# Kernel tuning notes

Measured on AMD Instinct MI355X. Metric: run time of the kernel, lower is better.

The kernel has to match this reference:

```python
import jax, jax.numpy as jnp
import numpy as np

D = 1024        # d_group
H = 8           # num_heads_group
WIN = 128       # attention window size
DH = D // H     # head_dim = 128
EPS = 1e-5


def _rmsnorm(x, scale):
    xf = x.astype(jnp.float32)
    var = jnp.mean(jnp.square(xf), axis=-1, keepdims=True)
    return (xf * jax.lax.rsqrt(var + EPS) * scale.astype(jnp.float32)).astype(x.dtype)


def _rope(x):
    # x: [B', S, H, Dh]
    S, Dh = x.shape[1], x.shape[3]
    freqs = 1.0 / (10000.0 ** (jnp.arange(0, Dh, 2, dtype=jnp.float32) / Dh))
    ang = jnp.arange(S, dtype=jnp.float32)[:, None] * freqs[None, :]  # [S, Dh/2]
    sin = jnp.repeat(jnp.sin(ang), 2, axis=-1)[None, :, None, :]
    cos = jnp.repeat(jnp.cos(ang), 2, axis=-1)[None, :, None, :]
    x1, x2 = jnp.split(x, 2, axis=-1)
    rot = jnp.concatenate([-x2, x1], axis=-1)
    return x * cos + rot * sin


def setup_inputs() -> dict:
    key = jax.random.key(0)
    ks = jax.random.split(key, 16)
    s = 0.02
    return {
        "group_x": jax.random.normal(ks[0], (8, 4096, D), jnp.float32),
        "context": jax.random.normal(ks[1], (8, D), jnp.float32),
        "W_ada": jax.random.normal(ks[2], (D, 6 * D), jnp.float32) * s,
        "b_ada": jnp.zeros((6 * D,), jnp.float32),
        "scale1": jnp.ones((D,), jnp.float32),
        "W_qkv": jax.random.normal(ks[3], (D, 3 * D), jnp.float32) * s,
        "b_qkv": jnp.zeros((3 * D,), jnp.float32),
        "W_out": jax.random.normal(ks[4], (D, D), jnp.float32) * s,
        "b_out": jnp.zeros((D,), jnp.float32),
        "scale2": jnp.ones((D,), jnp.float32),
        "W_ff1": jax.random.normal(ks[5], (D, 4 * D), jnp.float32) * s,
        "b_ff1": jnp.zeros((4 * D,), jnp.float32),
        "W_ff2": jax.random.normal(ks[6], (4 * D, D), jnp.float32) * s,
        "b_ff2": jnp.zeros((D,), jnp.float32),
    }


def reference(group_x, context, W_ada, b_ada, scale1, W_qkv, b_qkv, W_out, b_out,
              scale2, W_ff1, b_ff1, W_ff2, b_ff2):
    B, L, _ = group_x.shape
    nw = L // WIN

    # adaLN modulation params from context
    ada = jax.nn.silu(context) @ W_ada + b_ada              # [B, 6D]
    sh_msa, sc_msa, g_msa, sh_mlp, sc_mlp, g_mlp = jnp.split(ada, 6, axis=-1)
    sh_msa, sc_msa, g_msa = sh_msa[:, None], sc_msa[:, None], g_msa[:, None]
    sh_mlp, sc_mlp, g_mlp = sh_mlp[:, None], sc_mlp[:, None], g_mlp[:, None]

    # --- attention branch ---
    res = group_x
    x = _rmsnorm(group_x, scale1)
    x = x * (1 + sc_msa) + sh_msa
    xw = x.reshape(B * nw, WIN, D)
    qkv = xw @ W_qkv + b_qkv
    q, k, v = jnp.split(qkv, 3, axis=-1)
    q = _rope(q.reshape(B * nw, WIN, H, DH))
    k = _rope(k.reshape(B * nw, WIN, H, DH))
    v = v.reshape(B * nw, WIN, H, DH)
    scores = jnp.einsum('bqhd,bkhd->bhqk', q, k) / jnp.sqrt(jnp.float32(DH))
    attn = jax.nn.softmax(scores, axis=-1)
    o = jnp.einsum('bhqk,bkhd->bqhd', attn, v).reshape(B, L, D)
    o = o @ W_out + b_out
    x = res + g_msa * o

    # --- MLP branch ---
    res = x
    h = _rmsnorm(x, scale2)
    h = h * (1 + sc_mlp) + sh_mlp
    h = jax.nn.gelu(h @ W_ff1 + b_ff1)
    h = h @ W_ff2 + b_ff2
    return res + g_mlp * h
```

## Files before the change

### kernel.cpp

```cpp
#include <hip/hip_runtime.h>
#include <cstdint>
#include <cstddef>

typedef __bf16 bf16;
typedef __bf16 bf16x2 __attribute__((ext_vector_type(2)));
typedef __bf16 bf16x4 __attribute__((ext_vector_type(4)));
typedef __bf16 bf16x8 __attribute__((ext_vector_type(8)));
typedef float f32x4 __attribute__((ext_vector_type(4)));

#define D_MODEL 1024
#define ADA_STRIDE 6144
#define ROWS_TOTAL 32768
#define EPS_RMS 1e-5f

__device__ __forceinline__ void gld16(const void* g, void* l) {
  __builtin_amdgcn_global_load_lds((const __attribute__((address_space(1))) void*)g,
                                   (__attribute__((address_space(3))) void*)l, 16, 0, 0);
}

__global__ void wconvert_t(const float* __restrict__ W, bf16* __restrict__ Wt,
                           int kbits, int N, int total) {
  int i = blockIdx.x * 256 + threadIdx.x;
  if (i >= total) return;
  int K = 1 << kbits;
  int k = i & (K - 1);
  int n = i >> kbits;
  Wt[i] = (bf16)W[(size_t)k * N + n];
}

__global__ void ada_gemm(const float* __restrict__ ctx, const float* __restrict__ W,
                         const float* __restrict__ bias, float* __restrict__ ada) {
  __shared__ float sc[D_MODEL];
  int b = blockIdx.y;
  int col = blockIdx.x * 256 + threadIdx.x;
  for (int j = threadIdx.x; j < D_MODEL; j += 256) {
    float x = ctx[b * D_MODEL + j];
    sc[j] = x / (1.f + __expf(-x));
  }
  __syncthreads();
  float acc = bias[col];
#pragma unroll 8
  for (int k = 0; k < D_MODEL; ++k)
    acc += sc[k] * W[(size_t)k * ADA_STRIDE + col];
  ada[b * ADA_STRIDE + col] = acc;
}

__global__ void rmsnorm_mod(const float* __restrict__ x, const float* __restrict__ scale,
                            const float* __restrict__ ada, int shOff, int scOff,
                            bf16* __restrict__ out) {
  int row = blockIdx.x;
  int b = row >> 12;
  int t = threadIdx.x;
  const float* xr = x + (size_t)row * D_MODEL;
  float4 v = ((const float4*)xr)[t];
  float ss = v.x * v.x + v.y * v.y + v.z * v.z + v.w * v.w;
#pragma unroll
  for (int m = 32; m >= 1; m >>= 1) ss += __shfl_xor(ss, m, 64);
  __shared__ float ws[4];
  if ((t & 63) == 0) ws[t >> 6] = ss;
  __syncthreads();
  float tot = ws[0] + ws[1] + ws[2] + ws[3];
  float rms = rsqrtf(tot * (1.f / D_MODEL) + EPS_RMS);
  const float* ab = ada + b * ADA_STRIDE;
  int d0 = t * 4;
  float vv[4] = {v.x, v.y, v.z, v.w};
  bf16x4 o4;
#pragma unroll
  for (int j = 0; j < 4; ++j) {
    int d = d0 + j;
    float y = vv[j] * rms * scale[d];
    y = y * (1.f + ab[scOff + d]) + ab[shOff + d];
    o4[j] = (bf16)y;
  }
  *(bf16x4*)(out + (size_t)row * D_MODEL + d0) = o4;
}

__global__ void rope_kernel(bf16* __restrict__ qk) {
  int gid = blockIdx.x * 256 + threadIdx.x;
  int t = gid >> 5, i = gid & 31;
  int pos = t & 127;
  float fl = __expf((float)i * -0.14391156831f);
  float al = (float)pos * fl, ah = al * 0.01f;
  float sl, cl, sh, ch;
  __sincosf(al, &sl, &cl);
  __sincosf(ah, &sh, &ch);
  bf16* row = qk + (size_t)t * 2048;
  int d0 = i * 2;
#pragma unroll
  for (int h8 = 0; h8 < 16; ++h8) {
    bf16* hp = row + h8 * 128;
    bf16x2 lo = *(bf16x2*)(hp + d0);
    bf16x2 hi = *(bf16x2*)(hp + 64 + d0);
    bf16x2 olo, ohi;
#pragma unroll
    for (int j = 0; j < 2; ++j) {
      float xl = (float)lo[j], xh = (float)hi[j];
      olo[j] = (bf16)(xl * cl - xh * sl);
      ohi[j] = (bf16)(xh * ch + xl * sh);
    }
    *(bf16x2*)(hp + d0) = olo;
    *(bf16x2*)(hp + 64 + d0) = ohi;
  }
}

#define GEMM_LDS 131072

#define VMWAIT(N) asm volatile("s_waitcnt vmcnt(" #N ")" ::: "memory")
#define PH_BAR() __builtin_amdgcn_s_barrier()
#define KT_DO(...) __VA_ARGS__
#define KT_SKIP(...)

#define READ_AE() { _Pragma("unroll") for (int m_ = 0; m_ < 4; ++m_) \
  _Pragma("unroll") for (int s_ = 0; s_ < 2; ++s_) \
    a[m_][s_] = *(const bf16x8*)(lds + cb + aRow + m_ * 2048 + (g0 ^ (s_ * 32))); }
#define READ_AO() { _Pragma("unroll") for (int m_ = 0; m_ < 4; ++m_) \
  _Pragma("unroll") for (int s_ = 0; s_ < 2; ++s_) \
    a[m_][s_] = *(const bf16x8*)(lds + cb + aRow + 1024 + m_ * 2048 + (g0 ^ (s_ * 32))); }
#define READ_BE() { _Pragma("unroll") for (int n_ = 0; n_ < 2; ++n_) \
  _Pragma("unroll") for (int s_ = 0; s_ < 2; ++s_) \
    be[n_][s_] = *(const bf16x8*)(lds + cb + bRow + n_ * 2048 + (g0 ^ (s_ * 32))); }
#define READ_BO() { _Pragma("unroll") for (int n_ = 0; n_ < 2; ++n_) \
  _Pragma("unroll") for (int s_ = 0; s_ < 2; ++s_) \
    bo[n_][s_] = *(const bf16x8*)(lds + cb + bRow + 1024 + n_ * 2048 + (g0 ^ (s_ * 32))); }

#define MMPH(MOFF, BREG, NOFF) { __builtin_amdgcn_s_setprio(1); \
  _Pragma("unroll") for (int m_ = 0; m_ < 4; ++m_) \
  _Pragma("unroll") for (int n_ = 0; n_ < 2; ++n_) \
  _Pragma("unroll") for (int s_ = 0; s_ < 2; ++s_) \
    acc[2 * m_ + (MOFF)][2 * n_ + (NOFF)] = __builtin_amdgcn_mfma_f32_16x16x32_bf16( \
        BREG[n_][s_], a[m_][s_], acc[2 * m_ + (MOFF)][2 * n_ + (NOFF)], 0, 0, 0); \
  __builtin_amdgcn_s_setprio(0); }

#define KTILE(W0, W1, W2, STG) { \
    VMWAIT(W0); PH_BAR(); \
    READ_AE(); READ_BE(); \
    STG(gld16(gA + ko2, ldAn); gld16(gA + ko2 + K8, ldAn + 512);) \
    MMPH(0, be, 0); \
    VMWAIT(W1); PH_BAR(); \
    READ_BO(); \
    STG(gld16(gB + ko2, ldBn); gld16(gB + ko2 + K8, ldBn + 512);) \
    MMPH(0, bo, 1); \
    VMWAIT(W2); PH_BAR(); \
    READ_AO(); \
    STG(gld16(gB + ko2 + K16, ldBn + 1024); gld16(gB + ko2 + K24, ldBn + 1536);) \
    MMPH(1, bo, 1); \
    PH_BAR(); \
    STG(gld16(gA + ko2 + K16, ldAn + 1024); gld16(gA + ko2 + K24, ldAn + 1536);) \
    MMPH(1, be, 0); \
  }

template <int EPI>
__global__ __launch_bounds__(512, 2) void gemm256(
    const bf16* __restrict__ A, const bf16* __restrict__ Bt,
    const float* __restrict__ bias, int M, int K, int N,
    bf16* __restrict__ outB, float* __restrict__ outF,
    const float* __restrict__ resid, const float* __restrict__ ada, int gOff) {
  extern __shared__ char smem_raw[];
  bf16* lds = (bf16*)smem_raw;
  const int tid = threadIdx.x;
  const int lane = tid & 63;
  const int wv = tid >> 6;
  const int wm = wv >> 2;
  const int wn = wv & 3;
  const int lm = lane & 15;
  const int quad = lane >> 4;

  const int MT = M >> 8, NT = N >> 8;
  const int nwg = MT * NT;
  const int bid = blockIdx.x;
  const int wgid = (bid & 7) * (nwg >> 3) + (bid >> 3);
  const int width = 8 * NT;
  const int gid = wgid / width;
  const int first = gid * 8;
  const int gsize = (MT - first < 8) ? (MT - first) : 8;
  const int inG = wgid % width;
  const int tileM = (first + inG % gsize) << 8;
  const int tileN = (inG / gsize) << 8;

  const int srow = 32 * (tid >> 6) + ((tid & 63) >> 3);
  const int xg = ((tid & 7) ^ ((tid >> 3) & 7)) * 8;
  const bf16* gA = A + (size_t)(tileM + srow) * K + xg;
  const bf16* gB = Bt + (size_t)(tileN + srow) * K + xg;
  const size_t K8 = (size_t)K * 8;
  const size_t K16 = K8 * 2, K24 = K8 * 3;
  bf16* ldA = lds + (tid >> 6) * 2048 + (tid & 63) * 8;
  bf16* ldB = ldA + 16384;

  f32x4 acc[8][4];
#pragma unroll
  for (int i = 0; i < 8; ++i)
#pragma unroll
    for (int j = 0; j < 4; ++j) acc[i][j] = (f32x4){0.f, 0.f, 0.f, 0.f};

  const int g0 = (quad ^ (lm & 7)) * 8;
  const int aRow = wm * 8192 + lm * 64;
  const int bRow = 16384 + wn * 4096 + lm * 64;

  bf16x8 a[4][2], be[2][2], bo[2][2];

  gld16(gA, ldA);        gld16(gA + K8, ldA + 512);
  gld16(gB, ldB);        gld16(gB + K8, ldB + 512);
  gld16(gB + K16, ldB + 1024); gld16(gB + K24, ldB + 1536);
  gld16(gA + K16, ldA + 1024); gld16(gA + K24, ldA + 1536);

  const int nt = K >> 6;
  int cb = 0;
  for (int t = 0; t < nt - 1; ++t) {
    bf16* ldAn = ldA + (cb ^ 32768);
    bf16* ldBn = ldB + (cb ^ 32768);
    const size_t ko2 = (size_t)(t + 1) * 64;
    KTILE(4, 4, 4, KT_DO)
    cb ^= 32768;
  }
  KTILE(4, 2, 0, KT_SKIP)

#pragma unroll
  for (int mi = 0; mi < 8; ++mi) {
    int grow = tileM + wm * 128 + mi * 16 + lm;
    int b = grow >> 12;
    float brow = (EPI == 4) ? bias[grow] : 0.f;
#pragma unroll
    for (int ni = 0; ni < 4; ++ni) {
      int col0 = tileN + wn * 64 + ni * 16 + quad * 4;
      size_t idx = (size_t)grow * N + col0;
      if (EPI == 0) {
        float4 b4 = *(const float4*)(bias + col0);
        float bb[4] = {b4.x, b4.y, b4.z, b4.w};
        bf16x4 o;
#pragma unroll
        for (int r = 0; r < 4; ++r) o[r] = (bf16)(acc[mi][ni][r] + bb[r]);
        *(bf16x4*)(outB + idx) = o;
      } else if (EPI == 4) {
        bf16x4 o;
#pragma unroll
        for (int r = 0; r < 4; ++r) o[r] = (bf16)(acc[mi][ni][r] + brow);
        *(bf16x4*)(outB + idx) = o;
      } else if (EPI == 1) {
        float4 b4 = *(const float4*)(bias + col0);
        float bb[4] = {b4.x, b4.y, b4.z, b4.w};
        bf16x4 o;
#pragma unroll
        for (int r = 0; r < 4; ++r) {
          float v = acc[mi][ni][r] + bb[r];
          float s2 = 1.5957691216057308f * (v + 0.044715f * v * v * v);
          o[r] = (bf16)(v / (1.f + __expf(-s2)));
        }
        *(bf16x4*)(outB + idx) = o;
      } else if (EPI == 2) {
        float4 b4 = *(const float4*)(bias + col0);
        float4 g4 = *(const float4*)(ada + b * ADA_STRIDE + gOff + col0);
        float4 r4 = *(const float4*)(resid + idx);
        float4 o4;
        o4.x = r4.x + g4.x * (acc[mi][ni][0] + b4.x);
        o4.y = r4.y + g4.y * (acc[mi][ni][1] + b4.y);
        o4.z = r4.z + g4.z * (acc[mi][ni][2] + b4.z);
        o4.w = r4.w + g4.w * (acc[mi][ni][3] + b4.w);
        *(float4*)(outF + idx) = o4;
      } else {
        float4 b4 = *(const float4*)(bias + col0);
        float4 g4 = *(const float4*)(ada + b * ADA_STRIDE + gOff + col0);
        float4 r4 = *(const float4*)(outF + idx);
        float4 o4;
        o4.x = r4.x + g4.x * (acc[mi][ni][0] + b4.x);
        o4.y = r4.y + g4.y * (acc[mi][ni][1] + b4.y);
        o4.z = r4.z + g4.z * (acc[mi][ni][2] + b4.z);
        o4.w = r4.w + g4.w * (acc[mi][ni][3] + b4.w);
        *(float4*)(outF + idx) = o4;
      }
    }
  }
}

#define ATTN_LDS 65536

__global__ __launch_bounds__(256, 2) void attn_kernel(
    const bf16* __restrict__ qk, const bf16* __restrict__ vt, bf16* __restrict__ o) {
  extern __shared__ char smem[];
  bf16* qbuf = (bf16*)smem;
  bf16* kbuf = qbuf + 128 * 128;
  const int tid = threadIdx.x;
  const int lane = tid & 63;
  const int wv = tid >> 6;
  const int lm = lane & 15;
  const int quad = lane >> 4;
  const int w = blockIdx.x >> 3;
  const int h = blockIdx.x & 7;
  const int wbase = w * 128;

#pragma unroll
  for (int it = 0; it < 8; ++it) {
    int c = it * 256 + tid;
    int r = c >> 4, gst = c & 15;
    int goff = (gst ^ (r & 15)) * 8;
    const bf16* rowp = qk + (size_t)(wbase + r) * 2048 + h * 128 + goff;
    gld16(rowp, qbuf + c * 8);
    gld16(rowp + 1024, kbuf + c * 8);
  }
  __syncthreads();

  const int wq0 = wv * 32;
  f32x4 accS[8][2];
#pragma unroll
  for (int mi = 0; mi < 8; ++mi)
#pragma unroll
    for (int ni = 0; ni < 2; ++ni) accS[mi][ni] = (f32x4){0.f, 0.f, 0.f, 0.f};

#pragma unroll
  for (int s = 0; s < 4; ++s) {
    bf16x8 bq[2], ak[8];
#pragma unroll
    for (int ni = 0; ni < 2; ++ni)
      bq[ni] = *(const bf16x8*)(qbuf + (wq0 + ni * 16 + lm) * 128 + ((s * 4 + quad) ^ lm) * 8);
#pragma unroll
    for (int mi = 0; mi < 8; ++mi)
      ak[mi] = *(const bf16x8*)(kbuf + (mi * 16 + lm) * 128 + ((s * 4 + quad) ^ lm) * 8);
#pragma unroll
    for (int mi = 0; mi < 8; ++mi)
#pragma unroll
      for (int ni = 0; ni < 2; ++ni)
        accS[mi][ni] = __builtin_amdgcn_mfma_f32_16x16x32_bf16(ak[mi], bq[ni], accS[mi][ni], 0, 0, 0);
  }

  const float scl = 0.08838834764831845f;
  float mx[2] = {-1e30f, -1e30f}, sm[2] = {0.f, 0.f};
#pragma unroll
  for (int mi = 0; mi < 8; ++mi)
#pragma unroll
    for (int ni = 0; ni < 2; ++ni)
#pragma unroll
      for (int r = 0; r < 4; ++r) {
        accS[mi][ni][r] *= scl;
        mx[ni] = fmaxf(mx[ni], accS[mi][ni][r]);
      }
#pragma unroll
  for (int ni = 0; ni < 2; ++ni) {
    mx[ni] = fmaxf(mx[ni], __shfl_xor(mx[ni], 16, 64));
    mx[ni] = fmaxf(mx[ni], __shfl_xor(mx[ni], 32, 64));
  }
#pragma unroll
  for (int mi = 0; mi < 8; ++mi)
#pragma unroll
    for (int ni = 0; ni < 2; ++ni)
#pragma unroll
      for (int r = 0; r < 4; ++r) {
        accS[mi][ni][r] = __expf(accS[mi][ni][r] - mx[ni]);
        sm[ni] += accS[mi][ni][r];
      }
#pragma unroll
  for (int ni = 0; ni < 2; ++ni) {
    sm[ni] += __shfl_xor(sm[ni], 16, 64);
    sm[ni] += __shfl_xor(sm[ni], 32, 64);
    sm[ni] = 1.f / sm[ni];
  }
  __syncthreads();

#pragma unroll
  for (int mi = 0; mi < 8; ++mi)
#pragma unroll
    for (int ni = 0; ni < 2; ++ni) {
      int q = wq0 + ni * 16 + lm;
      int gst = (mi * 2 + (quad >> 1)) ^ lm;
      bf16x4 pk;
#pragma unroll
      for (int r = 0; r < 4; ++r) pk[r] = (bf16)(accS[mi][ni][r] * sm[ni]);
      *(bf16x4*)(qbuf + q * 128 + gst * 8 + (quad & 1) * 4) = pk;
    }
#pragma unroll
  for (int it = 0; it < 8; ++it) {
    int c = it * 256 + tid;
    int r = c >> 4, gst = c & 15;
    gld16(vt + (size_t)(h * 128 + r) * 32768 + wbase + (gst ^ (r & 15)) * 8, kbuf + c * 8);
  }
  __syncthreads();

  f32x4 accO[2][8];
#pragma unroll
  for (int mi = 0; mi < 2; ++mi)
#pragma unroll
    for (int ni = 0; ni < 8; ++ni) accO[mi][ni] = (f32x4){0.f, 0.f, 0.f, 0.f};
#pragma unroll
  for (int s = 0; s < 4; ++s) {
    bf16x8 ap[2], bv[8];
#pragma unroll
    for (int mi = 0; mi < 2; ++mi)
      ap[mi] = *(const bf16x8*)(qbuf + (wq0 + mi * 16 + lm) * 128 + ((s * 4 + quad) ^ lm) * 8);
#pragma unroll
    for (int ni = 0; ni < 8; ++ni)
      bv[ni] = *(const bf16x8*)(kbuf + (ni * 16 + lm) * 128 + ((s * 4 + quad) ^ lm) * 8);
#pragma unroll
    for (int mi = 0; mi < 2; ++mi)
#pragma unroll
      for (int ni = 0; ni < 8; ++ni)
        accO[mi][ni] = __builtin_amdgcn_mfma_f32_16x16x32_bf16(ap[mi], bv[ni], accO[mi][ni], 0, 0, 0);
  }

#pragma unroll
  for (int mi = 0; mi < 2; ++mi)
#pragma unroll
    for (int ni = 0; ni < 8; ++ni) {
      int d = ni * 16 + lm;
#pragma unroll
      for (int r = 0; r < 4; ++r) {
        int q = wq0 + mi * 16 + quad * 4 + r;
        o[(size_t)(wbase + q) * 1024 + h * 128 + d] = (bf16)accO[mi][ni][r];
      }
    }
}

extern "C" void kernel_launch(void* const* d_in, const int* in_sizes, int n_in,
                              void* d_out, int out_size, void* d_ws, size_t ws_size,
                              hipStream_t stream) {
  const float* group_x = (const float*)d_in[0];
  const float* context = (const float*)d_in[1];
  const float* W_ada   = (const float*)d_in[2];
  const float* b_ada   = (const float*)d_in[3];
  const float* scale1  = (const float*)d_in[4];
  const float* W_qkv   = (const float*)d_in[5];
  const float* b_qkv   = (const float*)d_in[6];
  const float* W_out   = (const float*)d_in[7];
  const float* b_out   = (const float*)d_in[8];
  const float* scale2  = (const float*)d_in[9];
  const float* W_ff1   = (const float*)d_in[10];
  const float* b_ff1   = (const float*)d_in[11];
  const float* W_ff2   = (const float*)d_in[12];
  const float* b_ff2   = (const float*)d_in[13];
  float* out = (float*)d_out;

  char* ws = (char*)d_ws;
  float* ada   = (float*)ws;
  bf16* wqkv_t = (bf16*)(ws + 196608);
  bf16* wout_t = wqkv_t + (size_t)3072 * 1024;
  bf16* wff1_t = wout_t + (size_t)1024 * 1024;
  bf16* wff2_t = wff1_t + (size_t)4096 * 1024;
  bf16* bufX   = wff2_t + (size_t)1024 * 4096;
  bf16* qkvQK  = bufX + (size_t)ROWS_TOTAL * 1024;
  bf16* vtbuf  = qkvQK + (size_t)ROWS_TOTAL * 2048;
  bf16* h1     = qkvQK;

  wconvert_t<<<dim3(3072 * 1024 / 256), 256, 0, stream>>>(W_qkv, wqkv_t, 10, 3072, 3072 * 1024);
  wconvert_t<<<dim3(1024 * 1024 / 256), 256, 0, stream>>>(W_out, wout_t, 10, 1024, 1024 * 1024);
  wconvert_t<<<dim3(4096 * 1024 / 256), 256, 0, stream>>>(W_ff1, wff1_t, 10, 4096, 4096 * 1024);
  wconvert_t<<<dim3(1024 * 4096 / 256), 256, 0, stream>>>(W_ff2, wff2_t, 12, 1024, 1024 * 4096);

  ada_gemm<<<dim3(ADA_STRIDE / 256, 8), 256, 0, stream>>>(context, W_ada, b_ada, ada);

  rmsnorm_mod<<<ROWS_TOTAL, 256, 0, stream>>>(group_x, scale1, ada, 0, 1024, bufX);

  hipFuncSetAttribute(reinterpret_cast<const void*>(&gemm256<0>),
                      hipFuncAttributeMaxDynamicSharedMemorySize, GEMM_LDS);
  hipFuncSetAttribute(reinterpret_cast<const void*>(&gemm256<1>),
                      hipFuncAttributeMaxDynamicSharedMemorySize, GEMM_LDS);
  hipFuncSetAttribute(reinterpret_cast<const void*>(&gemm256<2>),
                      hipFuncAttributeMaxDynamicSharedMemorySize, GEMM_LDS);
  hipFuncSetAttribute(reinterpret_cast<const void*>(&gemm256<3>),
                      hipFuncAttributeMaxDynamicSharedMemorySize, GEMM_LDS);
  hipFuncSetAttribute(reinterpret_cast<const void*>(&gemm256<4>),
                      hipFuncAttributeMaxDynamicSharedMemorySize, GEMM_LDS);

  gemm256<0><<<dim3(128 * 8), 512, GEMM_LDS, stream>>>(
      bufX, wqkv_t, b_qkv, ROWS_TOTAL, 1024, 2048, qkvQK, nullptr, nullptr, nullptr, 0);

  gemm256<4><<<dim3(4 * 128), 512, GEMM_LDS, stream>>>(
      wqkv_t + (size_t)2048 * 1024, bufX, b_qkv + 2048, 1024, 1024, ROWS_TOTAL,
      vtbuf, nullptr, nullptr, nullptr, 0);

  rope_kernel<<<dim3(ROWS_TOTAL * 32 / 256), 256, 0, stream>>>(qkvQK);

  hipFuncSetAttribute(reinterpret_cast<const void*>(&attn_kernel),
                      hipFuncAttributeMaxDynamicSharedMemorySize, ATTN_LDS);
  attn_kernel<<<dim3(256 * 8), 256, ATTN_LDS, stream>>>(qkvQK, vtbuf, bufX);

  gemm256<2><<<dim3(128 * 4), 512, GEMM_LDS, stream>>>(
      bufX, wout_t, b_out, ROWS_TOTAL, 1024, 1024, nullptr, out, group_x, ada, 2048);

  rmsnorm_mod<<<ROWS_TOTAL, 256, 0, stream>>>(out, scale2, ada, 3072, 4096, bufX);

  gemm256<1><<<dim3(128 * 16), 512, GEMM_LDS, stream>>>(
      bufX, wff1_t, b_ff1, ROWS_TOTAL, 1024, 4096, h1, nullptr, nullptr, nullptr, 0);

  gemm256<3><<<dim3(128 * 4), 512, GEMM_LDS, stream>>>(
      h1, wff2_t, b_ff2, ROWS_TOTAL, 4096, 1024, nullptr, out, nullptr, ada, 5120);
}
```

Baseline: 1.424 ms.

## Make GEMM persistent with cross-tile prefetch overlapping epilogue

```diff
diff --git a/kernel.cpp b/kernel.cpp
--- a/kernel.cpp
+++ b/kernel.cpp
@@ -107,8 +107,6 @@
 
 #define VMWAIT(N) asm volatile("s_waitcnt vmcnt(" #N ")" ::: "memory")
 #define PH_BAR() __builtin_amdgcn_s_barrier()
-#define KT_DO(...) __VA_ARGS__
-#define KT_SKIP(...)
 
 #define READ_AE() { _Pragma("unroll") for (int m_ = 0; m_ < 4; ++m_) \
   _Pragma("unroll") for (int s_ = 0; s_ < 2; ++s_) \
@@ -131,89 +129,50 @@
         BREG[n_][s_], a[m_][s_], acc[2 * m_ + (MOFF)][2 * n_ + (NOFF)], 0, 0, 0); \
   __builtin_amdgcn_s_setprio(0); }
 
-#define KTILE(W0, W1, W2, STG) { \
+#define STG_A01() gld16(gAs + ko2, ldAn); gld16(gAs + ko2 + K8, ldAn + 512)
+#define STG_B01() gld16(gBs + ko2, ldBn); gld16(gBs + ko2 + K8, ldBn + 512)
+#define STG_B23() gld16(gBs + ko2 + K16, ldBn + 1024); gld16(gBs + ko2 + K24, ldBn + 1536)
+#define STG_A23() gld16(gAs + ko2 + K16, ldAn + 1024); gld16(gAs + ko2 + K24, ldAn + 1536)
+
+#define KTILE_BODY(W0, W1, W3, S0, S1, S2, S3) { \
+    READ_AE(); READ_BE(); \
+    S0; \
     VMWAIT(W0); PH_BAR(); \
-    READ_AE(); READ_BE(); \
-    STG(gld16(gA + ko2, ldAn); gld16(gA + ko2 + K8, ldAn + 512);) \
     MMPH(0, be, 0); \
+    PH_BAR(); \
+    READ_BO(); \
+    S1; \
     VMWAIT(W1); PH_BAR(); \
-    READ_BO(); \
-    STG(gld16(gB + ko2, ldBn); gld16(gB + ko2 + K8, ldBn + 512);) \
     MMPH(0, bo, 1); \
-    VMWAIT(W2); PH_BAR(); \
+    PH_BAR(); \
     READ_AO(); \
-    STG(gld16(gB + ko2 + K16, ldBn + 1024); gld16(gB + ko2 + K24, ldBn + 1536);) \
+    S2; \
+    PH_BAR(); \
     MMPH(1, bo, 1); \
     PH_BAR(); \
-    STG(gld16(gA + ko2 + K16, ldAn + 1024); gld16(gA + ko2 + K24, ldAn + 1536);) \
+    S3; \
+    VMWAIT(W3); PH_BAR(); \
     MMPH(1, be, 0); \
-  }
+    PH_BAR(); \
+  }
+
+__device__ __forceinline__ void decode_tile(int vb, int nwg, int MT, int NT,
+                                            int& tileM, int& tileN) {
+  int wgid = (vb & 7) * (nwg >> 3) + (vb >> 3);
+  int width = 8 * NT;
+  int gid = wgid / width;
+  int first = gid * 8;
+  int gsize = (MT - first < 8) ? (MT - first) : 8;
+  int inG = wgid % width;
+  tileM = (first + inG % gsize) << 8;
+  tileN = (inG / gsize) << 8;
+}
 
 template <int EPI>
-__global__ __launch_bounds__(512, 2) void gemm256(
-    const bf16* __restrict__ A, const bf16* __restrict__ Bt,
-    const float* __restrict__ bias, int M, int K, int N,
-    bf16* __restrict__ outB, float* __restrict__ outF,
+__device__ __forceinline__ void epilogue256(
+    f32x4 (&acc)[8][4], int tileM, int tileN, int N, int wm, int wn, int lm, int quad,
+    const float* __restrict__ bias, bf16* __restrict__ outB, float* __restrict__ outF,
     const float* __restrict__ resid, const float* __restrict__ ada, int gOff) {
-  extern __shared__ char smem_raw[];
-  bf16* lds = (bf16*)smem_raw;
-  const int tid = threadIdx.x;
-  const int lane = tid & 63;
-  const int wv = tid >> 6;
-  const int wm = wv >> 2;
-  const int wn = wv & 3;
-  const int lm = lane & 15;
-  const int quad = lane >> 4;
-
-  const int MT = M >> 8, NT = N >> 8;
-  const int nwg = MT * NT;
-  const int bid = blockIdx.x;
-  const int wgid = (bid & 7) * (nwg >> 3) + (bid >> 3);
-  const int width = 8 * NT;
-  const int gid = wgid / width;
-  const int first = gid * 8;
-  const int gsize = (MT - first < 8) ? (MT - first) : 8;
-  const int inG = wgid % width;
-  const int tileM = (first + inG % gsize) << 8;
-  const int tileN = (inG / gsize) << 8;
-
-  const int srow = 32 * (tid >> 6) + ((tid & 63) >> 3);
-  const int xg = ((tid & 7) ^ ((tid >> 3) & 7)) * 8;
-  const bf16* gA = A + (size_t)(tileM + srow) * K + xg;
-  const bf16* gB = Bt + (size_t)(tileN + srow) * K + xg;
-  const size_t K8 = (size_t)K * 8;
-  const size_t K16 = K8 * 2, K24 = K8 * 3;
-  bf16* ldA = lds + (tid >> 6) * 2048 + (tid & 63) * 8;
-  bf16* ldB = ldA + 16384;
-
-  f32x4 acc[8][4];
-#pragma unroll
-  for (int i = 0; i < 8; ++i)
-#pragma unroll
-    for (int j = 0; j < 4; ++j) acc[i][j] = (f32x4){0.f, 0.f, 0.f, 0.f};
-
-  const int g0 = (quad ^ (lm & 7)) * 8;
-  const int aRow = wm * 8192 + lm * 64;
-  const int bRow = 16384 + wn * 4096 + lm * 64;
-
-  bf16x8 a[4][2], be[2][2], bo[2][2];
-
-  gld16(gA, ldA);        gld16(gA + K8, ldA + 512);
-  gld16(gB, ldB);        gld16(gB + K8, ldB + 512);
-  gld16(gB + K16, ldB + 1024); gld16(gB + K24, ldB + 1536);
-  gld16(gA + K16, ldA + 1024); gld16(gA + K24, ldA + 1536);
-
-  const int nt = K >> 6;
-  int cb = 0;
-  for (int t = 0; t < nt - 1; ++t) {
-    bf16* ldAn = ldA + (cb ^ 32768);
-    bf16* ldBn = ldB + (cb ^ 32768);
-    const size_t ko2 = (size_t)(t + 1) * 64;
-    KTILE(4, 4, 4, KT_DO)
-    cb ^= 32768;
-  }
-  KTILE(4, 2, 0, KT_SKIP)
-
 #pragma unroll
   for (int mi = 0; mi < 8; ++mi) {
     int grow = tileM + wm * 128 + mi * 16 + lm;
@@ -271,6 +230,100 @@
   }
 }
 
+template <int EPI>
+__global__ __launch_bounds__(512, 2) void gemm256(
+    const bf16* __restrict__ A, const bf16* __restrict__ Bt,
+    const float* __restrict__ bias, int M, int K, int N,
+    bf16* __restrict__ outB, float* __restrict__ outF,
+    const float* __restrict__ resid, const float* __restrict__ ada, int gOff) {
+  extern __shared__ char smem_raw[];
+  bf16* lds = (bf16*)smem_raw;
+  const int tid = threadIdx.x;
+  const int lane = tid & 63;
+  const int wv = tid >> 6;
+  const int wm = wv >> 2;
+  const int wn = wv & 3;
+  const int lm = lane & 15;
+  const int quad = lane >> 4;
+
+  const int MT = M >> 8, NT = N >> 8;
+  const int nwg = MT * NT;
+  const int nt = K >> 6;
+
+  int vb = blockIdx.x;
+  int tileM, tileN;
+  decode_tile(vb, nwg, MT, NT, tileM, tileN);
+
+  const int srow = 32 * wv + (lane >> 3);
+  const int xg = ((tid & 7) ^ ((tid >> 3) & 7)) * 8;
+  const size_t K8 = (size_t)K * 8;
+  const size_t K16 = K8 * 2, K24 = K8 * 3;
+  const bf16* gA = A + (size_t)(tileM + srow) * K + xg;
+  const bf16* gB = Bt + (size_t)(tileN + srow) * K + xg;
+  bf16* ldA = lds + wv * 2048 + lane * 8;
+  bf16* ldB = ldA + 16384;
+
+  const int g0 = (quad ^ (lm & 7)) * 8;
+  const int aRow = wm * 8192 + lm * 64;
+  const int bRow = 16384 + wn * 4096 + lm * 64;
+
+  f32x4 acc[8][4];
+  bf16x8 a[4][2], be[2][2], bo[2][2];
+
+  {
+    const bf16* gAs = gA; const bf16* gBs = gB;
+    bf16* ldAn = ldA; bf16* ldBn = ldB;
+    const size_t ko2 = 0;
+    STG_A01(); STG_B01(); STG_B23(); STG_A23();
+  }
+  VMWAIT(4);
+  PH_BAR();
+
+  int cb = 0;
+  for (;;) {
+#pragma unroll
+    for (int i = 0; i < 8; ++i)
+#pragma unroll
+      for (int j = 0; j < 4; ++j) acc[i][j] = (f32x4){0.f, 0.f, 0.f, 0.f};
+
+    const int vnext = vb + 256;
+    const bool more = vnext < nwg;
+
+    for (int t = 0; t < nt - 1; ++t) {
+      const bf16* gAs = gA; const bf16* gBs = gB;
+      bf16* ldAn = ldA + (cb ^ 32768);
+      bf16* ldBn = ldB + (cb ^ 32768);
+      const size_t ko2 = (size_t)(t + 1) * 64;
+      KTILE_BODY(4, 4, 4, STG_A01(), STG_B01(), STG_B23(), STG_A23())
+      cb ^= 32768;
+    }
+
+    if (more) {
+      int tileM2, tileN2;
+      decode_tile(vnext, nwg, MT, NT, tileM2, tileN2);
+      const bf16* gA2 = A + (size_t)(tileM2 + srow) * K + xg;
+      const bf16* gB2 = Bt + (size_t)(tileN2 + srow) * K + xg;
+      {
+        const bf16* gAs = gA2; const bf16* gBs = gB2;
+        bf16* ldAn = ldA + (cb ^ 32768);
+        bf16* ldBn = ldB + (cb ^ 32768);
+        const size_t ko2 = 0;
+        KTILE_BODY(4, 4, 4, STG_A01(), STG_B01(), STG_B23(), STG_A23())
+      }
+      cb ^= 32768;
+      epilogue256<EPI>(acc, tileM, tileN, N, wm, wn, lm, quad,
+                       bias, outB, outF, resid, ada, gOff);
+      vb = vnext; tileM = tileM2; tileN = tileN2; gA = gA2; gB = gB2;
+    } else {
+      KTILE_BODY(2, 0, 0, , , , )
+      cb ^= 32768;
+      epilogue256<EPI>(acc, tileM, tileN, N, wm, wn, lm, quad,
+                       bias, outB, outF, resid, ada, gOff);
+      break;
+    }
+  }
+}
+
 #define ATTN_LDS 65536
 
 __global__ __launch_bounds__(256, 2) void attn_kernel(
@@ -457,10 +510,10 @@
   hipFuncSetAttribute(reinterpret_cast<const void*>(&gemm256<4>),
                       hipFuncAttributeMaxDynamicSharedMemorySize, GEMM_LDS);
 
-  gemm256<0><<<dim3(128 * 8), 512, GEMM_LDS, stream>>>(
+  gemm256<0><<<dim3(256), 512, GEMM_LDS, stream>>>(
       bufX, wqkv_t, b_qkv, ROWS_TOTAL, 1024, 2048, qkvQK, nullptr, nullptr, nullptr, 0);
 
-  gemm256<4><<<dim3(4 * 128), 512, GEMM_LDS, stream>>>(
+  gemm256<4><<<dim3(256), 512, GEMM_LDS, stream>>>(
       wqkv_t + (size_t)2048 * 1024, bufX, b_qkv + 2048, 1024, 1024, ROWS_TOTAL,
       vtbuf, nullptr, nullptr, nullptr, 0);
 
@@ -470,14 +523,14 @@
                       hipFuncAttributeMaxDynamicSharedMemorySize, ATTN_LDS);
   attn_kernel<<<dim3(256 * 8), 256, ATTN_LDS, stream>>>(qkvQK, vtbuf, bufX);
 
-  gemm256<2><<<dim3(128 * 4), 512, GEMM_LDS, stream>>>(
+  gemm256<2><<<dim3(256), 512, GEMM_LDS, stream>>>(
       bufX, wout_t, b_out, ROWS_TOTAL, 1024, 1024, nullptr, out, group_x, ada, 2048);
 
   rmsnorm_mod<<<ROWS_TOTAL, 256, 0, stream>>>(out, scale2, ada, 3072, 4096, bufX);
 
-  gemm256<1><<<dim3(128 * 16), 512, GEMM_LDS, stream>>>(
+  gemm256<1><<<dim3(256), 512, GEMM_LDS, stream>>>(
       bufX, wff1_t, b_ff1, ROWS_TOTAL, 1024, 4096, h1, nullptr, nullptr, nullptr, 0);
 
-  gemm256<3><<<dim3(128 * 4), 512, GEMM_LDS, stream>>>(
+  gemm256<3><<<dim3(256), 512, GEMM_LDS, stream>>>(
       h1, wff2_t, b_ff2, ROWS_TOTAL, 4096, 1024, nullptr, out, nullptr, ada, 5120);
 }
```

Measured after the change: 1.489 ms. 1.05x slower.

## Halve barriers per k-tile in the bf16 GEMM by double-buffering A fragments

Applied to the files above, without the earlier changes.

```diff
diff --git a/kernel.cpp b/kernel.cpp
--- a/kernel.cpp
+++ b/kernel.cpp
@@ -107,15 +107,13 @@
 
 #define VMWAIT(N) asm volatile("s_waitcnt vmcnt(" #N ")" ::: "memory")
 #define PH_BAR() __builtin_amdgcn_s_barrier()
-#define KT_DO(...) __VA_ARGS__
-#define KT_SKIP(...)
 
 #define READ_AE() { _Pragma("unroll") for (int m_ = 0; m_ < 4; ++m_) \
   _Pragma("unroll") for (int s_ = 0; s_ < 2; ++s_) \
-    a[m_][s_] = *(const bf16x8*)(lds + cb + aRow + m_ * 2048 + (g0 ^ (s_ * 32))); }
+    ae[m_][s_] = *(const bf16x8*)(lds + cb + aRow + m_ * 2048 + (g0 ^ (s_ * 32))); }
 #define READ_AO() { _Pragma("unroll") for (int m_ = 0; m_ < 4; ++m_) \
   _Pragma("unroll") for (int s_ = 0; s_ < 2; ++s_) \
-    a[m_][s_] = *(const bf16x8*)(lds + cb + aRow + 1024 + m_ * 2048 + (g0 ^ (s_ * 32))); }
+    ao[m_][s_] = *(const bf16x8*)(lds + cb + aRow + 1024 + m_ * 2048 + (g0 ^ (s_ * 32))); }
 #define READ_BE() { _Pragma("unroll") for (int n_ = 0; n_ < 2; ++n_) \
   _Pragma("unroll") for (int s_ = 0; s_ < 2; ++s_) \
     be[n_][s_] = *(const bf16x8*)(lds + cb + bRow + n_ * 2048 + (g0 ^ (s_ * 32))); }
@@ -123,31 +121,18 @@
   _Pragma("unroll") for (int s_ = 0; s_ < 2; ++s_) \
     bo[n_][s_] = *(const bf16x8*)(lds + cb + bRow + 1024 + n_ * 2048 + (g0 ^ (s_ * 32))); }
 
-#define MMPH(MOFF, BREG, NOFF) { __builtin_amdgcn_s_setprio(1); \
+#define MMPH(AREG, MOFF, BREG, NOFF) { __builtin_amdgcn_s_setprio(1); \
   _Pragma("unroll") for (int m_ = 0; m_ < 4; ++m_) \
   _Pragma("unroll") for (int n_ = 0; n_ < 2; ++n_) \
   _Pragma("unroll") for (int s_ = 0; s_ < 2; ++s_) \
     acc[2 * m_ + (MOFF)][2 * n_ + (NOFF)] = __builtin_amdgcn_mfma_f32_16x16x32_bf16( \
-        BREG[n_][s_], a[m_][s_], acc[2 * m_ + (MOFF)][2 * n_ + (NOFF)], 0, 0, 0); \
+        BREG[n_][s_], AREG[m_][s_], acc[2 * m_ + (MOFF)][2 * n_ + (NOFF)], 0, 0, 0); \
   __builtin_amdgcn_s_setprio(0); }
 
-#define KTILE(W0, W1, W2, STG) { \
-    VMWAIT(W0); PH_BAR(); \
-    READ_AE(); READ_BE(); \
-    STG(gld16(gA + ko2, ldAn); gld16(gA + ko2 + K8, ldAn + 512);) \
-    MMPH(0, be, 0); \
-    VMWAIT(W1); PH_BAR(); \
-    READ_BO(); \
-    STG(gld16(gB + ko2, ldBn); gld16(gB + ko2 + K8, ldBn + 512);) \
-    MMPH(0, bo, 1); \
-    VMWAIT(W2); PH_BAR(); \
-    READ_AO(); \
-    STG(gld16(gB + ko2 + K16, ldBn + 1024); gld16(gB + ko2 + K24, ldBn + 1536);) \
-    MMPH(1, bo, 1); \
-    PH_BAR(); \
-    STG(gld16(gA + ko2 + K16, ldAn + 1024); gld16(gA + ko2 + K24, ldAn + 1536);) \
-    MMPH(1, be, 0); \
-  }
+#define STAGE_E() { gld16(gA + ko2, ldAn); gld16(gA + ko2 + K8, ldAn + 512); \
+                    gld16(gB + ko2, ldBn); gld16(gB + ko2 + K8, ldBn + 512); }
+#define STAGE_O() { gld16(gB + ko2 + K16, ldBn + 1024); gld16(gB + ko2 + K24, ldBn + 1536); \
+                    gld16(gA + ko2 + K16, ldAn + 1024); gld16(gA + ko2 + K24, ldAn + 1536); }
 
 template <int EPI>
 __global__ __launch_bounds__(512, 2) void gemm256(
@@ -177,31 +162,33 @@
   const int tileM = (first + inG % gsize) << 8;
   const int tileN = (inG / gsize) << 8;
 
-  const int srow = 32 * (tid >> 6) + ((tid & 63) >> 3);
+  const int srow = 32 * wv + (lane >> 3);
   const int xg = ((tid & 7) ^ ((tid >> 3) & 7)) * 8;
+  const size_t K8 = (size_t)K * 8;
+  const size_t K16 = K8 * 2, K24 = K8 * 3;
   const bf16* gA = A + (size_t)(tileM + srow) * K + xg;
   const bf16* gB = Bt + (size_t)(tileN + srow) * K + xg;
-  const size_t K8 = (size_t)K * 8;
-  const size_t K16 = K8 * 2, K24 = K8 * 3;
-  bf16* ldA = lds + (tid >> 6) * 2048 + (tid & 63) * 8;
+  bf16* ldA = lds + wv * 2048 + lane * 8;
   bf16* ldB = ldA + 16384;
-
-  f32x4 acc[8][4];
-#pragma unroll
-  for (int i = 0; i < 8; ++i)
-#pragma unroll
-    for (int j = 0; j < 4; ++j) acc[i][j] = (f32x4){0.f, 0.f, 0.f, 0.f};
 
   const int g0 = (quad ^ (lm & 7)) * 8;
   const int aRow = wm * 8192 + lm * 64;
   const int bRow = 16384 + wn * 4096 + lm * 64;
 
-  bf16x8 a[4][2], be[2][2], bo[2][2];
-
-  gld16(gA, ldA);        gld16(gA + K8, ldA + 512);
-  gld16(gB, ldB);        gld16(gB + K8, ldB + 512);
-  gld16(gB + K16, ldB + 1024); gld16(gB + K24, ldB + 1536);
-  gld16(gA + K16, ldA + 1024); gld16(gA + K24, ldA + 1536);
+  f32x4 acc[8][4];
+#pragma unroll
+  for (int i = 0; i < 8; ++i)
+#pragma unroll
+    for (int j = 0; j < 4; ++j) acc[i][j] = (f32x4){0.f, 0.f, 0.f, 0.f};
+
+  bf16x8 ae[4][2], ao[4][2], be[2][2], bo[2][2];
+
+  {
+    bf16* ldAn = ldA; bf16* ldBn = ldB;
+    const size_t ko2 = 0;
+    STAGE_E();
+    STAGE_O();
+  }
 
   const int nt = K >> 6;
   int cb = 0;
@@ -209,10 +196,28 @@
     bf16* ldAn = ldA + (cb ^ 32768);
     bf16* ldBn = ldB + (cb ^ 32768);
     const size_t ko2 = (size_t)(t + 1) * 64;
-    KTILE(4, 4, 4, KT_DO)
+    VMWAIT(4); PH_BAR();
+    READ_AE(); READ_BE();
+    STAGE_E();
+    MMPH(ae, 0, be, 0);
+    VMWAIT(4); PH_BAR();
+    READ_BO(); READ_AO();
+    STAGE_O();
+    MMPH(ae, 0, bo, 1);
+    MMPH(ao, 1, bo, 1);
+    MMPH(ao, 1, be, 0);
     cb ^= 32768;
   }
-  KTILE(4, 2, 0, KT_SKIP)
+  {
+    VMWAIT(4); PH_BAR();
+    READ_AE(); READ_BE();
+    MMPH(ae, 0, be, 0);
+    VMWAIT(0); PH_BAR();
+    READ_BO(); READ_AO();
+    MMPH(ae, 0, bo, 1);
+    MMPH(ao, 1, bo, 1);
+    MMPH(ao, 1, be, 0);
+  }
 
 #pragma unroll
   for (int mi = 0; mi < 8; ++mi) {
```

Result: no change. 1.423 ms (-0.1%).
